# Kernel tuning notes

Measured on AMD Instinct MI355X. Metric: run time of the kernel, lower is better.

The kernel has to match this reference:

```python
import jax, jax.numpy as jnp
import numpy as np

N = 50000        # nodes (users + candidates)
E = 1_600_000    # edges (interactions), avg degree 32
IN = 128         # in_channels
OUT = 128        # out_channels (GRU hidden)
HEAD = 16        # final linear head


def setup_inputs() -> dict:
    key = jax.random.key(0)
    ks = jax.random.split(key, 16)
    sx = 1.0 / np.sqrt(IN)
    sh = 1.0 / np.sqrt(OUT)
    return {
        "x": jax.random.normal(ks[0], (N, IN), jnp.float32),
        "edge_index": jax.random.randint(ks[1], (2, E), 0, N, dtype=jnp.int64),
        "edge_weight": jax.random.uniform(ks[2], (E,), jnp.float32),
        # graph-conv GRU gate weights (update z, reset r, candidate h)
        "W_xz": jax.random.normal(ks[3], (IN, OUT), jnp.float32) * sx,
        "W_hz": jax.random.normal(ks[4], (OUT, OUT), jnp.float32) * sh,
        "b_z": jnp.zeros((OUT,), jnp.float32),
        "W_xr": jax.random.normal(ks[5], (IN, OUT), jnp.float32) * sx,
        "W_hr": jax.random.normal(ks[6], (OUT, OUT), jnp.float32) * sh,
        "b_r": jnp.zeros((OUT,), jnp.float32),
        "W_xh": jax.random.normal(ks[7], (IN, OUT), jnp.float32) * sx,
        "W_hh": jax.random.normal(ks[8], (OUT, OUT), jnp.float32) * sh,
        "b_h": jnp.zeros((OUT,), jnp.float32),
        # final linear head: Linear(out_channels, 16)
        "W_lin": jax.random.normal(ks[9], (OUT, HEAD), jnp.float32) * sh,
        "b_lin": jnp.zeros((HEAD,), jnp.float32),
    }


def reference(x, edge_index, edge_weight,
              W_xz, W_hz, b_z, W_xr, W_hr, b_r, W_xh, W_hh, b_h,
              W_lin, b_lin):
    src, dst = edge_index[0], edge_index[1]

    # symmetric degree normalization from edge weights
    deg_out = jax.ops.segment_sum(edge_weight, src, num_segments=N)
    deg_in = jax.ops.segment_sum(edge_weight, dst, num_segments=N)
    inv_sqrt_out = jnp.where(deg_out > 0, 1.0 / jnp.sqrt(deg_out), 0.0)
    inv_sqrt_in = jnp.where(deg_in > 0, 1.0 / jnp.sqrt(deg_in), 0.0)
    norm = edge_weight * inv_sqrt_out[src] * inv_sqrt_in[dst]  # [E]

    def gconv(feat, W):
        # GCN-style conv: normalized weighted scatter-sum of transformed feats
        m = feat @ W                                   # [N, OUT]
        msg = m[src] * norm[:, None]                   # [E, OUT] gather
        return jax.ops.segment_sum(msg, dst, num_segments=N)  # scatter

    h = jnp.zeros((N, OUT), x.dtype)  # initial recurrent hidden state

    # GRU with graph-conv gates (GConvGRU-style recurrent cell)
    z = jax.nn.sigmoid(gconv(x, W_xz) + gconv(h, W_hz) + b_z)
    r = jax.nn.sigmoid(gconv(x, W_xr) + gconv(h, W_hr) + b_r)
    h_tilde = jnp.tanh(gconv(x, W_xh) + gconv(r * h, W_hh) + b_h)
    h_new = z * h + (1.0 - z) * h_tilde               # [N, OUT]

    return h_new @ W_lin + b_lin                       # [N, 16]
```

## Files before the change

### kernel.cpp

```cpp
#include <hip/hip_runtime.h>
#include <hip/hip_bf16.h>
#include <hip/hip_fp16.h>


#define CH 128
#define HEADS 16
#define TM 64
#define KC 32
#define DRANGE 12800
#define DSLICES 64
#define RN 98
#define NR 512
#define NB 256
#define SCAP 3840

typedef _Float16 half8 __attribute__((ext_vector_type(8)));
typedef _Float16 half4v __attribute__((ext_vector_type(4)));
typedef float floatx4 __attribute__((ext_vector_type(4)));

__global__ __launch_bounds__(256) void k_deg(const int* __restrict__ src,
                                             const float* __restrict__ w,
                                             float* __restrict__ partial, int E) {
    __shared__ float h[DRANGE];
    const int r = blockIdx.x / DSLICES;
    const int sl = blockIdx.x % DSLICES;
    const int base = r * DRANGE;
    for (int i = threadIdx.x; i < DRANGE; i += 256) h[i] = 0.f;
    __syncthreads();
    const int per = (E + DSLICES - 1) / DSLICES;
    const int lo = sl * per;
    const int hi = min(lo + per, E);
    int e = lo + threadIdx.x * 4;
    for (; e + 3 < hi; e += 1024) {
        int4 s4 = *reinterpret_cast<const int4*>(src + e);
        float4 w4 = *reinterpret_cast<const float4*>(w + e);
        int a;
        a = s4.x - base; if ((unsigned)a < DRANGE) atomicAdd(&h[a], w4.x);
        a = s4.y - base; if ((unsigned)a < DRANGE) atomicAdd(&h[a], w4.y);
        a = s4.z - base; if ((unsigned)a < DRANGE) atomicAdd(&h[a], w4.z);
        a = s4.w - base; if ((unsigned)a < DRANGE) atomicAdd(&h[a], w4.w);
    }
    for (; e < hi; ++e) {
        int a = src[e] - base;
        if ((unsigned)a < DRANGE) atomicAdd(&h[a], w[e]);
    }
    __syncthreads();
    float* dstp = partial + ((size_t)r * DSLICES + sl) * DRANGE;
    for (int i = threadIdx.x; i < DRANGE; i += 256) dstp[i] = h[i];
}

__global__ __launch_bounds__(256) void k_degxc(const float* __restrict__ partial,
                                               const float* __restrict__ x,
                                               __half* __restrict__ xh, int n) {
    __shared__ float degl[256];
    const int bb = blockIdx.x * 256;
    const int t = threadIdx.x;
    int i = bb + t;
    if (i < n) {
        int r = i / DRANGE;
        int idx = i - r * DRANGE;
        const float* p = partial + (size_t)r * DSLICES * DRANGE + idx;
        float s = 0.f;
#pragma unroll 8
        for (int sl = 0; sl < DSLICES; ++sl) s += p[(size_t)sl * DRANGE];
        degl[t] = s;
    }
    __syncthreads();
#pragma unroll
    for (int g = 0; g < 16; ++g) {
        int ln = g * 16 + (t >> 4);
        int node = bb + ln;
        if (node >= n) break;
        int c8 = (t & 15) * 8;
        float dg = degl[ln];
        float sc = dg > 0.f ? rsqrtf(dg) : 0.f;
        float4 a = *reinterpret_cast<const float4*>(x + (size_t)node * CH + c8);
        float4 b = *reinterpret_cast<const float4*>(x + (size_t)node * CH + c8 + 4);
        __half2 h0 = __floats2half2_rn(a.x * sc, a.y * sc);
        __half2 h1 = __floats2half2_rn(a.z * sc, a.w * sc);
        __half2 h2 = __floats2half2_rn(b.x * sc, b.y * sc);
        __half2 h3 = __floats2half2_rn(b.z * sc, b.w * sc);
        uint4 packed = make_uint4(*(unsigned*)&h0, *(unsigned*)&h1, *(unsigned*)&h2, *(unsigned*)&h3);
        *reinterpret_cast<uint4*>(xh + (size_t)node * CH + c8) = packed;
    }
}

__global__ __launch_bounds__(256) void k_wcast(const float* __restrict__ Wxz,
                                               const float* __restrict__ Wxh,
                                               const float* __restrict__ Wlin,
                                               __half* __restrict__ WzT,
                                               __half* __restrict__ WhT,
                                               __half* __restrict__ WlT) {
    int i = blockIdx.x * 256 + threadIdx.x;
    if (i < CH * CH) {
        int nn = i >> 7, k = i & 127;
        WzT[i] = __float2half(Wxz[k * CH + nn]);
        WhT[i] = __float2half(Wxh[k * CH + nn]);
    } else if (i < CH * CH + HEADS * CH) {
        int j = i - CH * CH;
        int nn = j >> 7, k = j & 127;
        WlT[j] = __float2half(Wlin[k * HEADS + nn]);
    }
}

__global__ __launch_bounds__(256) void k_count(const int* __restrict__ dst,
                                               unsigned* __restrict__ counts, int E) {
    __shared__ unsigned h[NR];
    const int b = blockIdx.x;
    for (int i = threadIdx.x; i < NR; i += 256) h[i] = 0u;
    __syncthreads();
    const int per = (E + NB - 1) / NB;
    const int lo = b * per;
    const int hi = min(lo + per, E);
    for (int e = lo + threadIdx.x; e < hi; e += 256)
        atomicAdd(&h[dst[e] / RN], 1u);
    __syncthreads();
    for (int i = threadIdx.x; i < NR; i += 256) counts[(size_t)i * NB + b] = h[i];
}

__global__ __launch_bounds__(256) void k_scanR(unsigned* __restrict__ counts,
                                               unsigned* __restrict__ total) {
    __shared__ unsigned s[256];
    const int r = blockIdx.x;
    const int t = threadIdx.x;
    unsigned v = counts[(size_t)r * NB + t];
    s[t] = v;
    __syncthreads();
    for (int ofs = 1; ofs < 256; ofs <<= 1) {
        unsigned u = (t >= ofs) ? s[t - ofs] : 0u;
        __syncthreads();
        s[t] += u;
        __syncthreads();
    }
    counts[(size_t)r * NB + t] = s[t] - v;
    if (t == 255) total[r] = s[255];
}

__global__ __launch_bounds__(512) void k_scanT(const unsigned* __restrict__ total,
                                               unsigned* __restrict__ rbase,
                                               unsigned* __restrict__ node_off,
                                               int n, int E) {
    __shared__ unsigned s[NR];
    const int t = threadIdx.x;
    unsigned v = total[t];
    s[t] = v;
    __syncthreads();
    for (int ofs = 1; ofs < NR; ofs <<= 1) {
        unsigned u = (t >= ofs) ? s[t - ofs] : 0u;
        __syncthreads();
        s[t] += u;
        __syncthreads();
    }
    rbase[t] = s[t] - v;
    if (t == 0) node_off[n] = (unsigned)E;
}

__global__ __launch_bounds__(256) void k_part(const int* __restrict__ src,
                                              const int* __restrict__ dst,
                                              const float* __restrict__ w,
                                              const unsigned* __restrict__ counts,
                                              const unsigned* __restrict__ rbase,
                                              int2* __restrict__ rec2, int E) {
    __shared__ unsigned cursor[NR];
    const int b = blockIdx.x;
    for (int r = threadIdx.x; r < NR; r += 256)
        cursor[r] = rbase[r] + counts[(size_t)r * NB + b];
    __syncthreads();
    const int per = (E + NB - 1) / NB;
    const int lo = b * per;
    const int hi = min(lo + per, E);
    for (int e = lo + threadIdx.x; e < hi; e += 256) {
        int d = dst[e];
        int r = d / RN;
        int dl = d - r * RN;
        unsigned pos = atomicAdd(&cursor[r], 1u);
        rec2[pos] = make_int2(__float_as_int(w[e]), (dl << 16) | src[e]);
    }
}

__global__ __launch_bounds__(256) void k_sortR(const unsigned* __restrict__ rbase,
                                               const unsigned* __restrict__ total,
                                               const int2* __restrict__ rec2,
                                               unsigned* __restrict__ rec3,
                                               unsigned* __restrict__ node_off, int n) {
    __shared__ int2 stage[SCAP];
    __shared__ unsigned hist[RN];
    __shared__ unsigned curx[RN];
    const int r = blockIdx.x;
    const int bn = r * RN;
    if (bn >= n) return;
    const int rn = min(RN, n - bn);
    const unsigned gbase = rbase[r];
    const unsigned tot = total[r];

    for (int i = threadIdx.x; i < RN; i += 256) hist[i] = 0u;
    __syncthreads();
    for (unsigned i = threadIdx.x; i < tot; i += 256) {
        int2 v = rec2[gbase + i];
        if (i < SCAP) stage[i] = v;
        atomicAdd(&hist[v.y >> 16], 1u);
    }
    __syncthreads();
    if (threadIdx.x == 0) {
        unsigned run = 0;
        for (int j = 0; j < rn; ++j) {
            unsigned c = hist[j];
            hist[j] = run;
            curx[j] = run;
            run += c;
        }
    }
    __syncthreads();
    for (int j = threadIdx.x; j < rn; j += 256)
        node_off[bn + j] = gbase + hist[j];
    for (unsigned i = threadIdx.x; i < tot; i += 256) {
        int2 v = (i < SCAP) ? stage[i] : rec2[gbase + i];
        int dl = v.y >> 16;
        __half hw = __float2half(__int_as_float(v.x));
        unsigned packed = ((unsigned)__half_as_ushort(hw) << 16) | (unsigned)(v.y & 0xFFFF);
        unsigned pos = atomicAdd(&curx[dl], 1u);
        rec3[gbase + pos] = packed;
    }
}

__global__ __launch_bounds__(256) void k_gather5(const unsigned* __restrict__ off,
                                                 const unsigned* __restrict__ rec3,
                                                 const __half* __restrict__ xh,
                                                 __half* __restrict__ xaggh, int n) {
    int node = blockIdx.x * 8 + (threadIdx.x >> 5);
    if (node >= n) return;
    int lane = threadIdx.x & 31;
    const __half* xb = xh + lane * 4;
    unsigned i = off[node];
    unsigned end = off[node + 1];
    float acc0 = 0.f, acc1 = 0.f, acc2 = 0.f, acc3 = 0.f;
    float wsum = 0.f;
    for (; i + 8 <= end; i += 8) {
        unsigned r0 = rec3[i],     r1 = rec3[i + 1], r2 = rec3[i + 2], r3 = rec3[i + 3];
        unsigned r4 = rec3[i + 4], r5 = rec3[i + 5], r6 = rec3[i + 6], r7 = rec3[i + 7];
        half4v v0 = *reinterpret_cast<const half4v*>(xb + (size_t)(r0 & 0xFFFFu) * CH);
        half4v v1 = *reinterpret_cast<const half4v*>(xb + (size_t)(r1 & 0xFFFFu) * CH);
        half4v v2 = *reinterpret_cast<const half4v*>(xb + (size_t)(r2 & 0xFFFFu) * CH);
        half4v v3 = *reinterpret_cast<const half4v*>(xb + (size_t)(r3 & 0xFFFFu) * CH);
        half4v v4 = *reinterpret_cast<const half4v*>(xb + (size_t)(r4 & 0xFFFFu) * CH);
        half4v v5 = *reinterpret_cast<const half4v*>(xb + (size_t)(r5 & 0xFFFFu) * CH);
        half4v v6 = *reinterpret_cast<const half4v*>(xb + (size_t)(r6 & 0xFFFFu) * CH);
        half4v v7 = *reinterpret_cast<const half4v*>(xb + (size_t)(r7 & 0xFFFFu) * CH);
        float w0 = __half2float(__ushort_as_half((unsigned short)(r0 >> 16)));
        float w1 = __half2float(__ushort_as_half((unsigned short)(r1 >> 16)));
        float w2 = __half2float(__ushort_as_half((unsigned short)(r2 >> 16)));
        float w3 = __half2float(__ushort_as_half((unsigned short)(r3 >> 16)));
        float w4 = __half2float(__ushort_as_half((unsigned short)(r4 >> 16)));
        float w5 = __half2float(__ushort_as_half((unsigned short)(r5 >> 16)));
        float w6 = __half2float(__ushort_as_half((unsigned short)(r6 >> 16)));
        float w7 = __half2float(__ushort_as_half((unsigned short)(r7 >> 16)));
        wsum += ((w0 + w1) + (w2 + w3)) + ((w4 + w5) + (w6 + w7));
        acc0 = fmaf(w0, (float)v0[0], acc0); acc1 = fmaf(w0, (float)v0[1], acc1);
        acc2 = fmaf(w0, (float)v0[2], acc2); acc3 = fmaf(w0, (float)v0[3], acc3);
        acc0 = fmaf(w1, (float)v1[0], acc0); acc1 = fmaf(w1, (float)v1[1], acc1);
        acc2 = fmaf(w1, (float)v1[2], acc2); acc3 = fmaf(w1, (float)v1[3], acc3);
        acc0 = fmaf(w2, (float)v2[0], acc0); acc1 = fmaf(w2, (float)v2[1], acc1);
        acc2 = fmaf(w2, (float)v2[2], acc2); acc3 = fmaf(w2, (float)v2[3], acc3);
        acc0 = fmaf(w3, (float)v3[0], acc0); acc1 = fmaf(w3, (float)v3[1], acc1);
        acc2 = fmaf(w3, (float)v3[2], acc2); acc3 = fmaf(w3, (float)v3[3], acc3);
        acc0 = fmaf(w4, (float)v4[0], acc0); acc1 = fmaf(w4, (float)v4[1], acc1);
        acc2 = fmaf(w4, (float)v4[2], acc2); acc3 = fmaf(w4, (float)v4[3], acc3);
        acc0 = fmaf(w5, (float)v5[0], acc0); acc1 = fmaf(w5, (float)v5[1], acc1);
        acc2 = fmaf(w5, (float)v5[2], acc2); acc3 = fmaf(w5, (float)v5[3], acc3);
        acc0 = fmaf(w6, (float)v6[0], acc0); acc1 = fmaf(w6, (float)v6[1], acc1);
        acc2 = fmaf(w6, (float)v6[2], acc2); acc3 = fmaf(w6, (float)v6[3], acc3);
        acc0 = fmaf(w7, (float)v7[0], acc0); acc1 = fmaf(w7, (float)v7[1], acc1);
        acc2 = fmaf(w7, (float)v7[2], acc2); acc3 = fmaf(w7, (float)v7[3], acc3);
    }
    for (; i + 4 <= end; i += 4) {
        unsigned r0 = rec3[i], r1 = rec3[i + 1], r2 = rec3[i + 2], r3 = rec3[i + 3];
        half4v v0 = *reinterpret_cast<const half4v*>(xb + (size_t)(r0 & 0xFFFFu) * CH);
        half4v v1 = *reinterpret_cast<const half4v*>(xb + (size_t)(r1 & 0xFFFFu) * CH);
        half4v v2 = *reinterpret_cast<const half4v*>(xb + (size_t)(r2 & 0xFFFFu) * CH);
        half4v v3 = *reinterpret_cast<const half4v*>(xb + (size_t)(r3 & 0xFFFFu) * CH);
        float w0 = __half2float(__ushort_as_half((unsigned short)(r0 >> 16)));
        float w1 = __half2float(__ushort_as_half((unsigned short)(r1 >> 16)));
        float w2 = __half2float(__ushort_as_half((unsigned short)(r2 >> 16)));
        float w3 = __half2float(__ushort_as_half((unsigned short)(r3 >> 16)));
        wsum += (w0 + w1) + (w2 + w3);
        acc0 = fmaf(w0, (float)v0[0], acc0); acc1 = fmaf(w0, (float)v0[1], acc1);
        acc2 = fmaf(w0, (float)v0[2], acc2); acc3 = fmaf(w0, (float)v0[3], acc3);
        acc0 = fmaf(w1, (float)v1[0], acc0); acc1 = fmaf(w1, (float)v1[1], acc1);
        acc2 = fmaf(w1, (float)v1[2], acc2); acc3 = fmaf(w1, (float)v1[3], acc3);
        acc0 = fmaf(w2, (float)v2[0], acc0); acc1 = fmaf(w2, (float)v2[1], acc1);
        acc2 = fmaf(w2, (float)v2[2], acc2); acc3 = fmaf(w2, (float)v2[3], acc3);
        acc0 = fmaf(w3, (float)v3[0], acc0); acc1 = fmaf(w3, (float)v3[1], acc1);
        acc2 = fmaf(w3, (float)v3[2], acc2); acc3 = fmaf(w3, (float)v3[3], acc3);
    }
    for (; i < end; ++i) {
        unsigned r0 = rec3[i];
        float w0 = __half2float(__ushort_as_half((unsigned short)(r0 >> 16)));
        half4v v0 = *reinterpret_cast<const half4v*>(xb + (size_t)(r0 & 0xFFFFu) * CH);
        wsum += w0;
        acc0 = fmaf(w0, (float)v0[0], acc0); acc1 = fmaf(w0, (float)v0[1], acc1);
        acc2 = fmaf(w0, (float)v0[2], acc2); acc3 = fmaf(w0, (float)v0[3], acc3);
    }
    float sc = wsum > 0.f ? rsqrtf(wsum) : 0.f;
    half4v hv;
    hv[0] = (_Float16)(acc0 * sc); hv[1] = (_Float16)(acc1 * sc);
    hv[2] = (_Float16)(acc2 * sc); hv[3] = (_Float16)(acc3 * sc);
    *reinterpret_cast<half4v*>(xaggh + (size_t)node * CH + lane * 4) = hv;
}

__global__ __launch_bounds__(256) void k_final3(const __half* __restrict__ xaggh,
                                                const __half* __restrict__ WzT,
                                                const __half* __restrict__ WhT,
                                                const __half* __restrict__ WlT,
                                                const float* __restrict__ bz,
                                                const float* __restrict__ bh,
                                                const float* __restrict__ blin,
                                                float* __restrict__ out, int n) {
    __shared__ __half gL[4][16][136];
    const int tid = threadIdx.x;
    const int w = tid >> 6;
    const int l = tid & 63;
    const int lr = l & 15;
    const int lk = l >> 4;
    const int nodeb = blockIdx.x * 64 + w * 16;

    int arow = nodeb + lr;
    if (arow > n - 1) arow = n - 1;

    floatx4 accz[8], acch[8];
#pragma unroll
    for (int ct = 0; ct < 8; ++ct) {
        accz[ct] = (floatx4){0.f, 0.f, 0.f, 0.f};
        acch[ct] = (floatx4){0.f, 0.f, 0.f, 0.f};
    }

#pragma unroll
    for (int kc = 0; kc < 4; ++kc) {
        half8 a = *reinterpret_cast<const half8*>(xaggh + (size_t)arow * CH + kc * 32 + lk * 8);
#pragma unroll
        for (int ct = 0; ct < 8; ++ct) {
            half8 bzf = *reinterpret_cast<const half8*>(WzT + (ct * 16 + lr) * CH + kc * 32 + lk * 8);
            accz[ct] = __builtin_amdgcn_mfma_f32_16x16x32_f16(a, bzf, accz[ct], 0, 0, 0);
            half8 bhf = *reinterpret_cast<const half8*>(WhT + (ct * 16 + lr) * CH + kc * 32 + lk * 8);
            acch[ct] = __builtin_amdgcn_mfma_f32_16x16x32_f16(a, bhf, acch[ct], 0, 0, 0);
        }
    }

#pragma unroll
    for (int ct = 0; ct < 8; ++ct) {
        float bzv = bz[ct * 16 + lr];
        float bhv = bh[ct * 16 + lr];
#pragma unroll
        for (int r = 0; r < 4; ++r) {
            float zp = accz[ct][r] + bzv;
            float hp = acch[ct][r] + bhv;
            float g = (1.f - 1.f / (1.f + __expf(-zp))) * tanhf(hp);
            gL[w][lk * 4 + r][ct * 16 + lr] = __float2half(g);
        }
    }
    __syncthreads();

    floatx4 acco = (floatx4){0.f, 0.f, 0.f, 0.f};
#pragma unroll
    for (int kc = 0; kc < 4; ++kc) {
        half8 a = *reinterpret_cast<const half8*>(&gL[w][lr][kc * 32 + lk * 8]);
        half8 b = *reinterpret_cast<const half8*>(WlT + lr * CH + kc * 32 + lk * 8);
        acco = __builtin_amdgcn_mfma_f32_16x16x32_f16(a, b, acco, 0, 0, 0);
    }
    float bl = blin[lr];
#pragma unroll
    for (int r = 0; r < 4; ++r) {
        int node = nodeb + lk * 4 + r;
        if (node < n) out[(size_t)node * HEADS + lr] = acco[r] + bl;
    }
}

__global__ __launch_bounds__(256) void k1B(const int* __restrict__ src,
                                           const int* __restrict__ dst,
                                           const float* __restrict__ w,
                                           float* __restrict__ deg_out,
                                           unsigned* __restrict__ cnt, int E) {
    int e = blockIdx.x * blockDim.x + threadIdx.x;
    if (e >= E) return;
    unsafeAtomicAdd(deg_out + src[e], w[e]);
    atomicAdd(cnt + dst[e], 1u);
}

__global__ __launch_bounds__(1024) void k_scan(unsigned* __restrict__ off, int n) {
    __shared__ unsigned s[1024];
    const int t = threadIdx.x;
    const int per = (n + 1023) / 1024;
    int lo = t * per;
    int hi = lo + per; if (hi > n) hi = n;
    unsigned sum = 0;
    for (int i = lo; i < hi; ++i) sum += off[i];
    s[t] = sum;
    __syncthreads();
    for (int ofs = 1; ofs < 1024; ofs <<= 1) {
        unsigned v = (t >= ofs) ? s[t - ofs] : 0u;
        __syncthreads();
        s[t] += v;
        __syncthreads();
    }
    unsigned run = s[t] - sum;
    for (int i = lo; i < hi; ++i) {
        unsigned c = off[i];
        off[i] = run;
        run += c;
    }
}

__global__ __launch_bounds__(256) void k_fillB(const int* __restrict__ src,
                                               const int* __restrict__ dst,
                                               const float* __restrict__ w,
                                               unsigned* __restrict__ off,
                                               int2* __restrict__ rec, int E) {
    int e = blockIdx.x * blockDim.x + threadIdx.x;
    if (e >= E) return;
    unsigned pos = atomicAdd(off + dst[e], 1u);
    rec[pos] = make_int2(__float_as_int(w[e]), src[e]);
}

__global__ __launch_bounds__(256) void k_gatherB(const unsigned* __restrict__ off,
                                                 const int2* __restrict__ rec,
                                                 const float* __restrict__ deg_out,
                                                 const float* __restrict__ x,
                                                 float* __restrict__ xagg, int n) {
    int node = blockIdx.x * 4 + (threadIdx.x >> 6);
    if (node >= n) return;
    int lane = threadIdx.x & 63;
    unsigned i = node ? off[node - 1] : 0u;
    unsigned end = off[node];
    float2 acc = make_float2(0.f, 0.f);
    float wsum = 0.f;
    for (; i < end; ++i) {
        int2 r0 = rec[i];
        float w0 = __int_as_float(r0.x);
        float d0 = deg_out[r0.y];
        float c0 = w0 * (d0 > 0.f ? rsqrtf(d0) : 0.f);
        float2 v = *reinterpret_cast<const float2*>(x + (size_t)r0.y * CH + lane * 2);
        wsum += w0;
        acc.x = fmaf(c0, v.x, acc.x);
        acc.y = fmaf(c0, v.y, acc.y);
    }
    float sc = wsum > 0.f ? rsqrtf(wsum) : 0.f;
    *reinterpret_cast<float2*>(xagg + (size_t)node * CH + lane * 2) =
        make_float2(acc.x * sc, acc.y * sc);
}

__global__ __launch_bounds__(256) void k_final2(const float* __restrict__ xagg,
                                                const float* __restrict__ Wxz,
                                                const float* __restrict__ bz,
                                                const float* __restrict__ Wxh,
                                                const float* __restrict__ bh,
                                                const float* __restrict__ Wlin,
                                                const float* __restrict__ blin,
                                                float* __restrict__ out, int n) {
    __shared__ float smem[10560];
    float* sA = smem;
    float* sWz = smem + 2304;
    float* sWh = smem + 6400;

    const int tid = threadIdx.x;
    const int tx = tid & 31;
    const int ty = tid >> 5;
    const int base = blockIdx.x * TM;

    float az[8][4] = {{0.f}};
    float ah[8][4] = {{0.f}};

    for (int kc = 0; kc < CH; kc += KC) {
        {
            int i = tid;
#pragma unroll
            for (int r2 = 0; r2 < 2; ++r2, i += 256) {
                int row = i >> 3;
                int c4 = (i & 7) * 4;
                int grow = base + row; if (grow > n - 1) grow = n - 1;
                float4 v = *reinterpret_cast<const float4*>(xagg + (size_t)grow * CH + kc + c4);
                *reinterpret_cast<float4*>(&sA[row * 36 + c4]) = v;
            }
            int j = tid;
#pragma unroll
            for (int r2 = 0; r2 < 4; ++r2, j += 256) {
                int row = j >> 5;
                int c4 = (j & 31) * 4;
                *reinterpret_cast<float4*>(&sWz[row * 128 + c4]) =
                    *reinterpret_cast<const float4*>(Wxz + (size_t)(kc + row) * CH + c4);
                *reinterpret_cast<float4*>(&sWh[row * 128 + c4]) =
                    *reinterpret_cast<const float4*>(Wxh + (size_t)(kc + row) * CH + c4);
            }
        }
        __syncthreads();
#pragma unroll 4
        for (int kk = 0; kk < KC; ++kk) {
            float4 wz = *reinterpret_cast<float4*>(&sWz[kk * 128 + tx * 4]);
            float4 wh = *reinterpret_cast<float4*>(&sWh[kk * 128 + tx * 4]);
#pragma unroll
            for (int r = 0; r < 8; ++r) {
                float a = sA[(ty * 8 + r) * 36 + kk];
                az[r][0] = fmaf(a, wz.x, az[r][0]);
                az[r][1] = fmaf(a, wz.y, az[r][1]);
                az[r][2] = fmaf(a, wz.z, az[r][2]);
                az[r][3] = fmaf(a, wz.w, az[r][3]);
                ah[r][0] = fmaf(a, wh.x, ah[r][0]);
                ah[r][1] = fmaf(a, wh.y, ah[r][1]);
                ah[r][2] = fmaf(a, wh.z, ah[r][2]);
                ah[r][3] = fmaf(a, wh.w, ah[r][3]);
            }
        }
        __syncthreads();
    }

    float* sG = smem;
    const float4 bz4 = *reinterpret_cast<const float4*>(bz + tx * 4);
    const float4 bh4 = *reinterpret_cast<const float4*>(bh + tx * 4);
#pragma unroll
    for (int r = 0; r < 8; ++r) {
        int row = ty * 8 + r;
        float4 g4;
        float zp = az[r][0] + bz4.x, hp = ah[r][0] + bh4.x;
        g4.x = (1.f - 1.f / (1.f + __expf(-zp))) * tanhf(hp);
        zp = az[r][1] + bz4.y; hp = ah[r][1] + bh4.y;
        g4.y = (1.f - 1.f / (1.f + __expf(-zp))) * tanhf(hp);
        zp = az[r][2] + bz4.z; hp = ah[r][2] + bh4.z;
        g4.z = (1.f - 1.f / (1.f + __expf(-zp))) * tanhf(hp);
        zp = az[r][3] + bz4.w; hp = ah[r][3] + bh4.w;
        g4.w = (1.f - 1.f / (1.f + __expf(-zp))) * tanhf(hp);
        *reinterpret_cast<float4*>(&sG[row * 132 + tx * 4]) = g4;
    }
    __syncthreads();

#pragma unroll
    for (int it = 0; it < 4; ++it) {
        int idx = it * 256 + tid;
        int node = idx >> 4;
        int hh = idx & 15;
        float acc = blin[hh];
#pragma unroll 8
        for (int j = 0; j < CH; ++j)
            acc = fmaf(sG[node * 132 + j], Wlin[j * HEADS + hh], acc);
        if (base + node < n) out[(size_t)(base + node) * HEADS + hh] = acc;
    }
}

static inline size_t align256(size_t v) { return (v + 255) & ~(size_t)255; }

extern "C" void kernel_launch(void* const* d_in, const int* in_sizes, int n_in,
                              void* d_out, int out_size, void* d_ws, size_t ws_size,
                              hipStream_t stream) {
    const float* x = (const float*)d_in[0];
    const int* ei = (const int*)d_in[1];
    const float* w = (const float*)d_in[2];
    const float* Wxz = (const float*)d_in[3];
    const float* bz = (const float*)d_in[5];
    const float* Wxh = (const float*)d_in[9];
    const float* bh = (const float*)d_in[11];
    const float* Wlin = (const float*)d_in[12];
    const float* blin = (const float*)d_in[13];
    float* out = (float*)d_out;

    const int Nn = in_sizes[0] / CH;
    const int E = in_sizes[2];

    const int* src = ei;
    const int* dst = ei + E;
    int eb = (E + 255) / 256;
    char* base = (char*)d_ws;

    size_t off_counts = 0;
    size_t off_total = align256(off_counts + (size_t)NR * NB * 4);
    size_t off_rbase = align256(off_total + NR * 4);
    size_t off_noff = align256(off_rbase + NR * 4);
    size_t off_xh = align256(off_noff + ((size_t)Nn + 1) * 4);
    size_t off_xaggh = align256(off_xh + (size_t)Nn * CH * 2);
    size_t off_wz = align256(off_xaggh + (size_t)Nn * CH * 2);
    size_t off_wh = align256(off_wz + (size_t)CH * CH * 2);
    size_t off_wl = align256(off_wh + (size_t)CH * CH * 2);
    size_t off_rec2 = align256(off_wl + (size_t)HEADS * CH * 2);
    size_t off_rec3 = align256(off_rec2 + (size_t)E * 8);
    size_t needNew = off_rec3 + (size_t)E * 4;
    size_t partial_bytes = (size_t)4 * DSLICES * DRANGE * 4;

    if (ws_size >= needNew && Nn <= 65536 && (size_t)NR * RN >= (size_t)Nn &&
        partial_bytes <= (size_t)E * 12) {
        unsigned* counts = (unsigned*)(base + off_counts);
        unsigned* total = (unsigned*)(base + off_total);
        unsigned* rbase = (unsigned*)(base + off_rbase);
        unsigned* noff = (unsigned*)(base + off_noff);
        __half* xh = (__half*)(base + off_xh);
        __half* xaggh = (__half*)(base + off_xaggh);
        __half* WzT = (__half*)(base + off_wz);
        __half* WhT = (__half*)(base + off_wh);
        __half* WlT = (__half*)(base + off_wl);
        int2* rec2 = (int2*)(base + off_rec2);
        unsigned* rec3 = (unsigned*)(base + off_rec3);
        float* partial = (float*)(base + off_rec2);

        k_deg<<<4 * DSLICES, 256, 0, stream>>>(src, w, partial, E);
        k_degxc<<<(Nn + 255) / 256, 256, 0, stream>>>(partial, x, xh, Nn);
        k_wcast<<<(CH * CH + HEADS * CH + 255) / 256, 256, 0, stream>>>(Wxz, Wxh, Wlin, WzT, WhT, WlT);
        k_count<<<NB, 256, 0, stream>>>(dst, counts, E);
        k_scanR<<<NR, 256, 0, stream>>>(counts, total);
        k_scanT<<<1, NR, 0, stream>>>(total, rbase, noff, Nn, E);
        k_part<<<NB, 256, 0, stream>>>(src, dst, w, counts, rbase, rec2, E);
        k_sortR<<<NR, 256, 0, stream>>>(rbase, total, rec2, rec3, noff, Nn);
        k_gather5<<<(Nn + 7) / 8, 256, 0, stream>>>(noff, rec3, xh, xaggh, Nn);
        k_final3<<<(Nn + 63) / 64, 256, 0, stream>>>(xaggh, WzT, WhT, WlT, bz, bh, blin, out, Nn);
    } else {
        unsigned* off = (unsigned*)base;
        float* deg_out = (float*)(base + (size_t)Nn * 4);
        int2* rec = (int2*)(base + (size_t)2 * Nn * 4);
        float* xagg = (float*)((char*)rec + (size_t)E * 8);

        hipMemsetAsync(d_ws, 0, (size_t)2 * Nn * 4, stream);
        k1B<<<eb, 256, 0, stream>>>(src, dst, w, deg_out, off, E);
        k_scan<<<1, 1024, 0, stream>>>(off, Nn);
        k_fillB<<<eb, 256, 0, stream>>>(src, dst, w, off, rec, E);
        k_gatherB<<<(Nn + 3) / 4, 256, 0, stream>>>(off, rec, deg_out, x, xagg, Nn);
        k_final2<<<(Nn + TM - 1) / TM, 256, 0, stream>>>(xagg, Wxz, bz, Wxh, bh, Wlin, blin, out, Nn);
    }
}
```

Before: 171.4 us.

## Fuse region sort with gather and fold scans and weight cast into neighbours

The weight-cast kernel is merged into the degree/x-cast kernel as extra blocks. The single-block total scan is removed, and each partition and sort block now redundantly recomputes the 512-entry prefix in shared memory. The per-region sort and the gather are fused into one 1024-thread kernel that keeps the sorted records in shared memory when a region fits, which skips the rec3 and node_off global round trip and cuts launches. The cost is lower gather parallelism per region, since there are 512 blocks of 32 half-warps, and larger shared-memory use that limits occupancy.

Measured after the change: 160.2 us. 1.07x faster.

```diff
diff --git a/kernel.cpp b/kernel.cpp
--- a/kernel.cpp
+++ b/kernel.cpp
@@ -49,12 +49,32 @@
     for (int i = threadIdx.x; i < DRANGE; i += 256) dstp[i] = h[i];
 }
 
-__global__ __launch_bounds__(256) void k_degxc(const float* __restrict__ partial,
-                                               const float* __restrict__ x,
-                                               __half* __restrict__ xh, int n) {
+__global__ __launch_bounds__(256) void k_degxcw(const float* __restrict__ partial,
+                                                const float* __restrict__ x,
+                                                __half* __restrict__ xh,
+                                                const float* __restrict__ Wxz,
+                                                const float* __restrict__ Wxh,
+                                                const float* __restrict__ Wlin,
+                                                __half* __restrict__ WzT,
+                                                __half* __restrict__ WhT,
+                                                __half* __restrict__ WlT,
+                                                int n, int nbdeg) {
+    const int t = threadIdx.x;
+    if ((int)blockIdx.x >= nbdeg) {
+        int i = (blockIdx.x - nbdeg) * 256 + t;
+        if (i < CH * CH) {
+            int nn = i >> 7, k = i & 127;
+            WzT[i] = __float2half(Wxz[k * CH + nn]);
+            WhT[i] = __float2half(Wxh[k * CH + nn]);
+        } else if (i < CH * CH + HEADS * CH) {
+            int j = i - CH * CH;
+            int nn = j >> 7, k = j & 127;
+            WlT[j] = __float2half(Wlin[k * HEADS + nn]);
+        }
+        return;
+    }
     __shared__ float degl[256];
     const int bb = blockIdx.x * 256;
-    const int t = threadIdx.x;
     int i = bb + t;
     if (i < n) {
         int r = i / DRANGE;
@@ -85,24 +105,6 @@
     }
 }
 
-__global__ __launch_bounds__(256) void k_wcast(const float* __restrict__ Wxz,
-                                               const float* __restrict__ Wxh,
-                                               const float* __restrict__ Wlin,
-                                               __half* __restrict__ WzT,
-                                               __half* __restrict__ WhT,
-                                               __half* __restrict__ WlT) {
-    int i = blockIdx.x * 256 + threadIdx.x;
-    if (i < CH * CH) {
-        int nn = i >> 7, k = i & 127;
-        WzT[i] = __float2half(Wxz[k * CH + nn]);
-        WhT[i] = __float2half(Wxh[k * CH + nn]);
-    } else if (i < CH * CH + HEADS * CH) {
-        int j = i - CH * CH;
-        int nn = j >> 7, k = j & 127;
-        WlT[j] = __float2half(Wlin[k * HEADS + nn]);
-    }
-}
-
 __global__ __launch_bounds__(256) void k_count(const int* __restrict__ dst,
                                                unsigned* __restrict__ counts, int E) {
     __shared__ unsigned h[NR];
@@ -136,40 +138,37 @@
     if (t == 255) total[r] = s[255];
 }
 
-__global__ __launch_bounds__(512) void k_scanT(const unsigned* __restrict__ total,
-                                               unsigned* __restrict__ rbase,
-                                               unsigned* __restrict__ node_off,
-                                               int n, int E) {
-    __shared__ unsigned s[NR];
-    const int t = threadIdx.x;
-    unsigned v = total[t];
-    s[t] = v;
-    __syncthreads();
-    for (int ofs = 1; ofs < NR; ofs <<= 1) {
-        unsigned u = (t >= ofs) ? s[t - ofs] : 0u;
-        __syncthreads();
-        s[t] += u;
-        __syncthreads();
-    }
-    rbase[t] = s[t] - v;
-    if (t == 0) node_off[n] = (unsigned)E;
-}
-
 __global__ __launch_bounds__(256) void k_part(const int* __restrict__ src,
                                               const int* __restrict__ dst,
                                               const float* __restrict__ w,
                                               const unsigned* __restrict__ counts,
-                                              const unsigned* __restrict__ rbase,
+                                              const unsigned* __restrict__ total,
                                               int2* __restrict__ rec2, int E) {
     __shared__ unsigned cursor[NR];
+    __shared__ unsigned sa[NR], sb[NR];
     const int b = blockIdx.x;
-    for (int r = threadIdx.x; r < NR; r += 256)
-        cursor[r] = rbase[r] + counts[(size_t)r * NB + b];
+    const int t = threadIdx.x;
+    sa[t] = total[t]; sa[t + 256] = total[t + 256];
+    __syncthreads();
+    unsigned* cur = sa; unsigned* nxt = sb;
+    for (int ofs = 1; ofs < NR; ofs <<= 1) {
+        for (int k = t; k < NR; k += 256) {
+            unsigned v = cur[k];
+            if (k >= ofs) v += cur[k - ofs];
+            nxt[k] = v;
+        }
+        __syncthreads();
+        unsigned* tmp = cur; cur = nxt; nxt = tmp;
+    }
+    for (int r = t; r < NR; r += 256) {
+        unsigned rb = cur[r] - total[r];
+        cursor[r] = rb + counts[(size_t)r * NB + b];
+    }
     __syncthreads();
     const int per = (E + NB - 1) / NB;
     const int lo = b * per;
     const int hi = min(lo + per, E);
-    for (int e = lo + threadIdx.x; e < hi; e += 256) {
+    for (int e = lo + t; e < hi; e += 256) {
         int d = dst[e];
         int r = d / RN;
         int dl = d - r * RN;
@@ -178,30 +177,45 @@
     }
 }
 
-__global__ __launch_bounds__(256) void k_sortR(const unsigned* __restrict__ rbase,
-                                               const unsigned* __restrict__ total,
-                                               const int2* __restrict__ rec2,
-                                               unsigned* __restrict__ rec3,
-                                               unsigned* __restrict__ node_off, int n) {
+__global__ __launch_bounds__(1024) void k_sortgather(const unsigned* __restrict__ total,
+                                                     const int2* __restrict__ rec2,
+                                                     unsigned* __restrict__ rec3,
+                                                     const __half* __restrict__ xh,
+                                                     __half* __restrict__ xaggh, int n) {
     __shared__ int2 stage[SCAP];
-    __shared__ unsigned hist[RN];
-    __shared__ unsigned curx[RN];
+    __shared__ unsigned sortedP[SCAP];
+    __shared__ unsigned hist[RN], curx[RN];
+    __shared__ unsigned sa[NR], sb[NR];
     const int r = blockIdx.x;
     const int bn = r * RN;
     if (bn >= n) return;
     const int rn = min(RN, n - bn);
-    const unsigned gbase = rbase[r];
+    const int t = threadIdx.x;
+
+    if (t < NR) sa[t] = total[t];
+    __syncthreads();
+    unsigned* cur = sa; unsigned* nxt = sb;
+    for (int ofs = 1; ofs < NR; ofs <<= 1) {
+        if (t < NR) {
+            unsigned v = cur[t];
+            if (t >= ofs) v += cur[t - ofs];
+            nxt[t] = v;
+        }
+        __syncthreads();
+        unsigned* tmp = cur; cur = nxt; nxt = tmp;
+    }
     const unsigned tot = total[r];
-
-    for (int i = threadIdx.x; i < RN; i += 256) hist[i] = 0u;
-    __syncthreads();
-    for (unsigned i = threadIdx.x; i < tot; i += 256) {
+    const unsigned gbase = cur[r] - tot;
+
+    if (t < RN) hist[t] = 0u;
+    __syncthreads();
+    for (unsigned i = t; i < tot; i += 1024) {
         int2 v = rec2[gbase + i];
         if (i < SCAP) stage[i] = v;
         atomicAdd(&hist[v.y >> 16], 1u);
     }
     __syncthreads();
-    if (threadIdx.x == 0) {
+    if (t == 0) {
         unsigned run = 0;
         for (int j = 0; j < rn; ++j) {
             unsigned c = hist[j];
@@ -211,100 +225,84 @@
         }
     }
     __syncthreads();
-    for (int j = threadIdx.x; j < rn; j += 256)
-        node_off[bn + j] = gbase + hist[j];
-    for (unsigned i = threadIdx.x; i < tot; i += 256) {
+    const bool big = (tot > SCAP);
+    for (unsigned i = t; i < tot; i += 1024) {
         int2 v = (i < SCAP) ? stage[i] : rec2[gbase + i];
         int dl = v.y >> 16;
         __half hw = __float2half(__int_as_float(v.x));
         unsigned packed = ((unsigned)__half_as_ushort(hw) << 16) | (unsigned)(v.y & 0xFFFF);
         unsigned pos = atomicAdd(&curx[dl], 1u);
-        rec3[gbase + pos] = packed;
-    }
-}
-
-__global__ __launch_bounds__(256) void k_gather5(const unsigned* __restrict__ off,
-                                                 const unsigned* __restrict__ rec3,
-                                                 const __half* __restrict__ xh,
-                                                 __half* __restrict__ xaggh, int n) {
-    int node = blockIdx.x * 8 + (threadIdx.x >> 5);
-    if (node >= n) return;
-    int lane = threadIdx.x & 31;
+        if (big) rec3[gbase + pos] = packed;
+        else sortedP[pos] = packed;
+    }
+    __syncthreads();
+
+    const int hwid = t >> 5;
+    const int lane = t & 31;
     const __half* xb = xh + lane * 4;
-    unsigned i = off[node];
-    unsigned end = off[node + 1];
-    float acc0 = 0.f, acc1 = 0.f, acc2 = 0.f, acc3 = 0.f;
-    float wsum = 0.f;
-    for (; i + 8 <= end; i += 8) {
-        unsigned r0 = rec3[i],     r1 = rec3[i + 1], r2 = rec3[i + 2], r3 = rec3[i + 3];
-        unsigned r4 = rec3[i + 4], r5 = rec3[i + 5], r6 = rec3[i + 6], r7 = rec3[i + 7];
-        half4v v0 = *reinterpret_cast<const half4v*>(xb + (size_t)(r0 & 0xFFFFu) * CH);
-        half4v v1 = *reinterpret_cast<const half4v*>(xb + (size_t)(r1 & 0xFFFFu) * CH);
-        half4v v2 = *reinterpret_cast<const half4v*>(xb + (size_t)(r2 & 0xFFFFu) * CH);
-        half4v v3 = *reinterpret_cast<const half4v*>(xb + (size_t)(r3 & 0xFFFFu) * CH);
-        half4v v4 = *reinterpret_cast<const half4v*>(xb + (size_t)(r4 & 0xFFFFu) * CH);
-        half4v v5 = *reinterpret_cast<const half4v*>(xb + (size_t)(r5 & 0xFFFFu) * CH);
-        half4v v6 = *reinterpret_cast<const half4v*>(xb + (size_t)(r6 & 0xFFFFu) * CH);
-        half4v v7 = *reinterpret_cast<const half4v*>(xb + (size_t)(r7 & 0xFFFFu) * CH);
-        float w0 = __half2float(__ushort_as_half((unsigned short)(r0 >> 16)));
-        float w1 = __half2float(__ushort_as_half((unsigned short)(r1 >> 16)));
-        float w2 = __half2float(__ushort_as_half((unsigned short)(r2 >> 16)));
-        float w3 = __half2float(__ushort_as_half((unsigned short)(r3 >> 16)));
-        float w4 = __half2float(__ushort_as_half((unsigned short)(r4 >> 16)));
-        float w5 = __half2float(__ushort_as_half((unsigned short)(r5 >> 16)));
-        float w6 = __half2float(__ushort_as_half((unsigned short)(r6 >> 16)));
-        float w7 = __half2float(__ushort_as_half((unsigned short)(r7 >> 16)));
-        wsum += ((w0 + w1) + (w2 + w3)) + ((w4 + w5) + (w6 + w7));
-        acc0 = fmaf(w0, (float)v0[0], acc0); acc1 = fmaf(w0, (float)v0[1], acc1);
-        acc2 = fmaf(w0, (float)v0[2], acc2); acc3 = fmaf(w0, (float)v0[3], acc3);
-        acc0 = fmaf(w1, (float)v1[0], acc0); acc1 = fmaf(w1, (float)v1[1], acc1);
-        acc2 = fmaf(w1, (float)v1[2], acc2); acc3 = fmaf(w1, (float)v1[3], acc3);
-        acc0 = fmaf(w2, (float)v2[0], acc0); acc1 = fmaf(w2, (float)v2[1], acc1);
-        acc2 = fmaf(w2, (float)v2[2], acc2); acc3 = fmaf(w2, (float)v2[3], acc3);
-        acc0 = fmaf(w3, (float)v3[0], acc0); acc1 = fmaf(w3, (float)v3[1], acc1);
-        acc2 = fmaf(w3, (float)v3[2], acc2); acc3 = fmaf(w3, (float)v3[3], acc3);
-        acc0 = fmaf(w4, (float)v4[0], acc0); acc1 = fmaf(w4, (float)v4[1], acc1);
-        acc2 = fmaf(w4, (float)v4[2], acc2); acc3 = fmaf(w4, (float)v4[3], acc3);
-        acc0 = fmaf(w5, (float)v5[0], acc0); acc1 = fmaf(w5, (float)v5[1], acc1);
-        acc2 = fmaf(w5, (float)v5[2], acc2); acc3 = fmaf(w5, (float)v5[3], acc3);
-        acc0 = fmaf(w6, (float)v6[0], acc0); acc1 = fmaf(w6, (float)v6[1], acc1);
-        acc2 = fmaf(w6, (float)v6[2], acc2); acc3 = fmaf(w6, (float)v6[3], acc3);
-        acc0 = fmaf(w7, (float)v7[0], acc0); acc1 = fmaf(w7, (float)v7[1], acc1);
-        acc2 = fmaf(w7, (float)v7[2], acc2); acc3 = fmaf(w7, (float)v7[3], acc3);
-    }
-    for (; i + 4 <= end; i += 4) {
-        unsigned r0 = rec3[i], r1 = rec3[i + 1], r2 = rec3[i + 2], r3 = rec3[i + 3];
-        half4v v0 = *reinterpret_cast<const half4v*>(xb + (size_t)(r0 & 0xFFFFu) * CH);
-        half4v v1 = *reinterpret_cast<const half4v*>(xb + (size_t)(r1 & 0xFFFFu) * CH);
-        half4v v2 = *reinterpret_cast<const half4v*>(xb + (size_t)(r2 & 0xFFFFu) * CH);
-        half4v v3 = *reinterpret_cast<const half4v*>(xb + (size_t)(r3 & 0xFFFFu) * CH);
-        float w0 = __half2float(__ushort_as_half((unsigned short)(r0 >> 16)));
-        float w1 = __half2float(__ushort_as_half((unsigned short)(r1 >> 16)));
-        float w2 = __half2float(__ushort_as_half((unsigned short)(r2 >> 16)));
-        float w3 = __half2float(__ushort_as_half((unsigned short)(r3 >> 16)));
-        wsum += (w0 + w1) + (w2 + w3);
-        acc0 = fmaf(w0, (float)v0[0], acc0); acc1 = fmaf(w0, (float)v0[1], acc1);
-        acc2 = fmaf(w0, (float)v0[2], acc2); acc3 = fmaf(w0, (float)v0[3], acc3);
-        acc0 = fmaf(w1, (float)v1[0], acc0); acc1 = fmaf(w1, (float)v1[1], acc1);
-        acc2 = fmaf(w1, (float)v1[2], acc2); acc3 = fmaf(w1, (float)v1[3], acc3);
-        acc0 = fmaf(w2, (float)v2[0], acc0); acc1 = fmaf(w2, (float)v2[1], acc1);
-        acc2 = fmaf(w2, (float)v2[2], acc2); acc3 = fmaf(w2, (float)v2[3], acc3);
-        acc0 = fmaf(w3, (float)v3[0], acc0); acc1 = fmaf(w3, (float)v3[1], acc1);
-        acc2 = fmaf(w3, (float)v3[2], acc2); acc3 = fmaf(w3, (float)v3[3], acc3);
-    }
-    for (; i < end; ++i) {
-        unsigned r0 = rec3[i];
-        float w0 = __half2float(__ushort_as_half((unsigned short)(r0 >> 16)));
-        half4v v0 = *reinterpret_cast<const half4v*>(xb + (size_t)(r0 & 0xFFFFu) * CH);
-        wsum += w0;
-        acc0 = fmaf(w0, (float)v0[0], acc0); acc1 = fmaf(w0, (float)v0[1], acc1);
-        acc2 = fmaf(w0, (float)v0[2], acc2); acc3 = fmaf(w0, (float)v0[3], acc3);
-    }
-    float sc = wsum > 0.f ? rsqrtf(wsum) : 0.f;
-    half4v hv;
-    hv[0] = (_Float16)(acc0 * sc); hv[1] = (_Float16)(acc1 * sc);
-    hv[2] = (_Float16)(acc2 * sc); hv[3] = (_Float16)(acc3 * sc);
-    *reinterpret_cast<half4v*>(xaggh + (size_t)node * CH + lane * 4) = hv;
+    const unsigned* grec = rec3 + gbase;
+    for (int nd = hwid; nd < rn; nd += 32) {
+        unsigned i = hist[nd];
+        unsigned end = curx[nd];
+        float acc0 = 0.f, acc1 = 0.f, acc2 = 0.f, acc3 = 0.f;
+        float wsum = 0.f;
+        for (; i + 8 <= end; i += 8) {
+            unsigned r0, r1, r2, r3, r4, r5, r6, r7;
+            if (big) {
+                r0 = grec[i];     r1 = grec[i + 1]; r2 = grec[i + 2]; r3 = grec[i + 3];
+                r4 = grec[i + 4]; r5 = grec[i + 5]; r6 = grec[i + 6]; r7 = grec[i + 7];
+            } else {
+                r0 = sortedP[i];     r1 = sortedP[i + 1]; r2 = sortedP[i + 2]; r3 = sortedP[i + 3];
+                r4 = sortedP[i + 4]; r5 = sortedP[i + 5]; r6 = sortedP[i + 6]; r7 = sortedP[i + 7];
+            }
+            half4v v0 = *reinterpret_cast<const half4v*>(xb + (size_t)(r0 & 0xFFFFu) * CH);
+            half4v v1 = *reinterpret_cast<const half4v*>(xb + (size_t)(r1 & 0xFFFFu) * CH);
+            half4v v2 = *reinterpret_cast<const half4v*>(xb + (size_t)(r2 & 0xFFFFu) * CH);
+            half4v v3 = *reinterpret_cast<const half4v*>(xb + (size_t)(r3 & 0xFFFFu) * CH);
+            half4v v4 = *reinterpret_cast<const half4v*>(xb + (size_t)(r4 & 0xFFFFu) * CH);
+            half4v v5 = *reinterpret_cast<const half4v*>(xb + (size_t)(r5 & 0xFFFFu) * CH);
+            half4v v6 = *reinterpret_cast<const half4v*>(xb + (size_t)(r6 & 0xFFFFu) * CH);
+            half4v v7 = *reinterpret_cast<const half4v*>(xb + (size_t)(r7 & 0xFFFFu) * CH);
+            float w0 = __half2float(__ushort_as_half((unsigned short)(r0 >> 16)));
+            float w1 = __half2float(__ushort_as_half((unsigned short)(r1 >> 16)));
+            float w2 = __half2float(__ushort_as_half((unsigned short)(r2 >> 16)));
+            float w3 = __half2float(__ushort_as_half((unsigned short)(r3 >> 16)));
+            float w4 = __half2float(__ushort_as_half((unsigned short)(r4 >> 16)));
+            float w5 = __half2float(__ushort_as_half((unsigned short)(r5 >> 16)));
+            float w6 = __half2float(__ushort_as_half((unsigned short)(r6 >> 16)));
+            float w7 = __half2float(__ushort_as_half((unsigned short)(r7 >> 16)));
+            wsum += ((w0 + w1) + (w2 + w3)) + ((w4 + w5) + (w6 + w7));
+            acc0 = fmaf(w0, (float)v0[0], acc0); acc1 = fmaf(w0, (float)v0[1], acc1);
+            acc2 = fmaf(w0, (float)v0[2], acc2); acc3 = fmaf(w0, (float)v0[3], acc3);
+            acc0 = fmaf(w1, (float)v1[0], acc0); acc1 = fmaf(w1, (float)v1[1], acc1);
+            acc2 = fmaf(w1, (float)v1[2], acc2); acc3 = fmaf(w1, (float)v1[3], acc3);
+            acc0 = fmaf(w2, (float)v2[0], acc0); acc1 = fmaf(w2, (float)v2[1], acc1);
+            acc2 = fmaf(w2, (float)v2[2], acc2); acc3 = fmaf(w2, (float)v2[3], acc3);
+            acc0 = fmaf(w3, (float)v3[0], acc0); acc1 = fmaf(w3, (float)v3[1], acc1);
+            acc2 = fmaf(w3, (float)v3[2], acc2); acc3 = fmaf(w3, (float)v3[3], acc3);
+            acc0 = fmaf(w4, (float)v4[0], acc0); acc1 = fmaf(w4, (float)v4[1], acc1);
+            acc2 = fmaf(w4, (float)v4[2], acc2); acc3 = fmaf(w4, (float)v4[3], acc3);
+            acc0 = fmaf(w5, (float)v5[0], acc0); acc1 = fmaf(w5, (float)v5[1], acc1);
+            acc2 = fmaf(w5, (float)v5[2], acc2); acc3 = fmaf(w5, (float)v5[3], acc3);
+            acc0 = fmaf(w6, (float)v6[0], acc0); acc1 = fmaf(w6, (float)v6[1], acc1);
+            acc2 = fmaf(w6, (float)v6[2], acc2); acc3 = fmaf(w6, (float)v6[3], acc3);
+            acc0 = fmaf(w7, (float)v7[0], acc0); acc1 = fmaf(w7, (float)v7[1], acc1);
+            acc2 = fmaf(w7, (float)v7[2], acc2); acc3 = fmaf(w7, (float)v7[3], acc3);
+        }
+        for (; i < end; ++i) {
+            unsigned r0 = big ? grec[i] : sortedP[i];
+            float w0 = __half2float(__ushort_as_half((unsigned short)(r0 >> 16)));
+            half4v v0 = *reinterpret_cast<const half4v*>(xb + (size_t)(r0 & 0xFFFFu) * CH);
+            wsum += w0;
+            acc0 = fmaf(w0, (float)v0[0], acc0); acc1 = fmaf(w0, (float)v0[1], acc1);
+            acc2 = fmaf(w0, (float)v0[2], acc2); acc3 = fmaf(w0, (float)v0[3], acc3);
+        }
+        float sc = wsum > 0.f ? rsqrtf(wsum) : 0.f;
+        half4v hv;
+        hv[0] = (_Float16)(acc0 * sc); hv[1] = (_Float16)(acc1 * sc);
+        hv[2] = (_Float16)(acc2 * sc); hv[3] = (_Float16)(acc3 * sc);
+        *reinterpret_cast<half4v*>(xaggh + (size_t)(bn + nd) * CH + lane * 4) = hv;
+    }
 }
 
 __global__ __launch_bounds__(256) void k_final3(const __half* __restrict__ xaggh,
@@ -569,9 +567,7 @@
 
     size_t off_counts = 0;
     size_t off_total = align256(off_counts + (size_t)NR * NB * 4);
-    size_t off_rbase = align256(off_total + NR * 4);
-    size_t off_noff = align256(off_rbase + NR * 4);
-    size_t off_xh = align256(off_noff + ((size_t)Nn + 1) * 4);
+    size_t off_xh = align256(off_total + NR * 4);
     size_t off_xaggh = align256(off_xh + (size_t)Nn * CH * 2);
     size_t off_wz = align256(off_xaggh + (size_t)Nn * CH * 2);
     size_t off_wh = align256(off_wz + (size_t)CH * CH * 2);
@@ -585,8 +581,6 @@
         partial_bytes <= (size_t)E * 12) {
         unsigned* counts = (unsigned*)(base + off_counts);
         unsigned* total = (unsigned*)(base + off_total);
-        unsigned* rbase = (unsigned*)(base + off_rbase);
-        unsigned* noff = (unsigned*)(base + off_noff);
         __half* xh = (__half*)(base + off_xh);
         __half* xaggh = (__half*)(base + off_xaggh);
         __half* WzT = (__half*)(base + off_wz);
@@ -596,15 +590,16 @@
         unsigned* rec3 = (unsigned*)(base + off_rec3);
         float* partial = (float*)(base + off_rec2);
 
+        int nbdeg = (Nn + 255) / 256;
+        int nbw = (CH * CH + HEADS * CH + 255) / 256;
+
         k_deg<<<4 * DSLICES, 256, 0, stream>>>(src, w, partial, E);
-        k_degxc<<<(Nn + 255) / 256, 256, 0, stream>>>(partial, x, xh, Nn);
-        k_wcast<<<(CH * CH + HEADS * CH + 255) / 256, 256, 0, stream>>>(Wxz, Wxh, Wlin, WzT, WhT, WlT);
+        k_degxcw<<<nbdeg + nbw, 256, 0, stream>>>(partial, x, xh, Wxz, Wxh, Wlin,
+                                                  WzT, WhT, WlT, Nn, nbdeg);
         k_count<<<NB, 256, 0, stream>>>(dst, counts, E);
         k_scanR<<<NR, 256, 0, stream>>>(counts, total);
-        k_scanT<<<1, NR, 0, stream>>>(total, rbase, noff, Nn, E);
-        k_part<<<NB, 256, 0, stream>>>(src, dst, w, counts, rbase, rec2, E);
-        k_sortR<<<NR, 256, 0, stream>>>(rbase, total, rec2, rec3, noff, Nn);
-        k_gather5<<<(Nn + 7) / 8, 256, 0, stream>>>(noff, rec3, xh, xaggh, Nn);
+        k_part<<<NB, 256, 0, stream>>>(src, dst, w, counts, total, rec2, E);
+        k_sortgather<<<NR, 1024, 0, stream>>>(total, rec2, rec3, xh, xaggh, Nn);
         k_final3<<<(Nn + 63) / 64, 256, 0, stream>>>(xaggh, WzT, WhT, WlT, bz, bh, blin, out, Nn);
     } else {
         unsigned* off = (unsigned*)base;
```
